# Kernel tuning notes

Measured on AMD Instinct MI355X. Metric: run time of the kernel, lower is better.

Reference implementation:

```python
import jax, jax.numpy as jnp
import numpy as np

B, TQ, TK = 4, 256, 256
Q, K, H = 256, 256, 256


def setup_inputs() -> dict:
    key = jax.random.key(0)
    ks = jax.random.split(key, 10)
    s = 0.05
    return {
        "queries": jax.random.normal(ks[0], (B, TQ, Q), dtype=jnp.float32),
        "keys": jax.random.normal(ks[1], (B, TK, K), dtype=jnp.float32),
        # lengths in [T//2, T] so no fully-masked query rows (torch would NaN there too)
        "query_lengths": jax.random.randint(ks[2], (B,), TQ // 2, TQ + 1),
        "key_lengths": jax.random.randint(ks[3], (B,), TK // 2, TK + 1),
        # nn.Linear(Q+K, H): weight applied as x @ W1; torch concat order is [keys, queries]
        "W1": jax.random.normal(ks[4], (K + Q, H), dtype=jnp.float32) * s,
        "b1": jax.random.normal(ks[5], (H,), dtype=jnp.float32) * s,
        "W2": jax.random.normal(ks[6], (H, H), dtype=jnp.float32) * s,
        "b2": jax.random.normal(ks[7], (H,), dtype=jnp.float32) * s,
        "W3": jax.random.normal(ks[8], (H, 1), dtype=jnp.float32) * s,
        "b3": jax.random.normal(ks[9], (1,), dtype=jnp.float32) * s,
    }


def reference(queries, keys, query_lengths, key_lengths, W1, b1, W2, b2, W3, b3):
    Bn, Tq, Qd = queries.shape
    Tk, Kd = keys.shape[1], keys.shape[2]
    # Split the first linear: concat([keys, queries]) @ W1 == keys@W1[:K] + queries@W1[K:]
    kh = jnp.einsum("bkd,dh->bkh", keys, W1[:Kd])      # [B,Tk,H]
    qh = jnp.einsum("bqd,dh->bqh", queries, W1[Kd:])   # [B,Tq,H]
    h = jax.nn.relu(qh[:, :, None, :] + kh[:, None, :, :] + b1)  # [B,Tq,Tk,H]
    h = jax.nn.relu(jnp.einsum("bqkh,hg->bqkg", h, W2) + b2)     # [B,Tq,Tk,H]
    scores = jnp.einsum("bqkh,h->bqk", h, W3[:, 0]) + b3[0]       # [B,Tq,Tk]
    # mask True where position is padding (query OR key out of range)
    mask = (jnp.arange(Tq)[None, :, None] >= query_lengths[:, None, None]) | (
        jnp.arange(Tk)[None, None, :] >= key_lengths[:, None, None]
    )
    scores = jnp.where(mask, -1e30, scores)
    probs = jax.nn.softmax(scores, axis=-1)
    probs = jnp.where(mask, 0.0, probs)
    return jnp.einsum("bqk,bkd->bqd", probs, keys)  # [B,Tq,K]
```

## Files before the change

### kernel.cpp

```cpp
#include <hip/hip_runtime.h>
#include <cstdint>

#define BATCH 4
#define TQ 256
#define TK 256
#define DIM 256
#define HD 256

typedef _Float16 f16x8 __attribute__((ext_vector_type(8)));
typedef float f32x4 __attribute__((ext_vector_type(4)));

union U4H8 { uint4 u; f16x8 v; };

#define KEEP(x) asm volatile("" : "+v"(x))

__device__ __forceinline__ unsigned short f2h(float f) {
    _Float16 h = (_Float16)f;
    unsigned short u;
    __builtin_memcpy(&u, &h, 2);
    return u;
}

__device__ __forceinline__ uint32_t pk2h(float a, float b) {
    auto r = __builtin_amdgcn_cvt_pkrtz(a, b);
    uint32_t w;
    __builtin_memcpy(&w, &r, 4);
    return w;
}

__global__ __launch_bounds__(256) void prep_all(
    const float* __restrict__ queries, const float* __restrict__ keys,
    const float* __restrict__ W1, const float* __restrict__ b1,
    const float* __restrict__ W2,
    float* __restrict__ qh, float* __restrict__ kh,
    unsigned short* __restrict__ W2T) {
    int i = blockIdx.x;
    int t = threadIdx.x;
    if (i >= 512) {
        __shared__ float tile[32][33];
        int bi = i - 512;
        int tx = t & 31, ty = t >> 5;
        int tc = (bi & 7) * 32, tn = (bi >> 3) * 32;
#pragma unroll
        for (int r = 0; r < 4; ++r)
            tile[ty + r * 8][tx] = W2[(tc + ty + r * 8) * HD + tn + tx];
        __syncthreads();
#pragma unroll
        for (int r = 0; r < 4; ++r)
            W2T[(tn + ty + r * 8) * HD + tc + tx] = f2h(tile[tx][ty + r * 8]);
        return;
    }
    bool isQ = i < 256;
    int r0 = (i & 255) * 4;
    const float* X = isQ ? queries : keys;
    const float* W = W1 + (isQ ? DIM * HD : 0);
    float* O = isQ ? qh : kh;
    __shared__ float4 xs4[4][DIM / 4];
    xs4[t >> 6][t & 63] =
        *(const float4*)(X + (size_t)(r0 + (t >> 6)) * DIM + (t & 63) * 4);
    __syncthreads();
    float acc[4] = {0.f, 0.f, 0.f, 0.f};
#pragma unroll 4
    for (int d4 = 0; d4 < DIM / 4; ++d4) {
        const float4 x0 = xs4[0][d4];
        const float4 x1 = xs4[1][d4];
        const float4 x2 = xs4[2][d4];
        const float4 x3 = xs4[3][d4];
        const float w0 = W[(d4 * 4 + 0) * HD + t];
        const float w1 = W[(d4 * 4 + 1) * HD + t];
        const float w2 = W[(d4 * 4 + 2) * HD + t];
        const float w3 = W[(d4 * 4 + 3) * HD + t];
        acc[0] = fmaf(x0.x, w0, acc[0]); acc[1] = fmaf(x1.x, w0, acc[1]);
        acc[2] = fmaf(x2.x, w0, acc[2]); acc[3] = fmaf(x3.x, w0, acc[3]);
        acc[0] = fmaf(x0.y, w1, acc[0]); acc[1] = fmaf(x1.y, w1, acc[1]);
        acc[2] = fmaf(x2.y, w1, acc[2]); acc[3] = fmaf(x3.y, w1, acc[3]);
        acc[0] = fmaf(x0.z, w2, acc[0]); acc[1] = fmaf(x1.z, w2, acc[1]);
        acc[2] = fmaf(x2.z, w2, acc[2]); acc[3] = fmaf(x3.z, w2, acc[3]);
        acc[0] = fmaf(x0.w, w3, acc[0]); acc[1] = fmaf(x1.w, w3, acc[1]);
        acc[2] = fmaf(x2.w, w3, acc[2]); acc[3] = fmaf(x3.w, w3, acc[3]);
    }
    float bias = isQ ? b1[t] : 0.f;
#pragma unroll
    for (int r = 0; r < 4; ++r) O[(size_t)(r0 + r) * HD + t] = acc[r] + bias;
}

__global__ __launch_bounds__(256, 2) void mlp_attn(
    const float* __restrict__ qh, const float* __restrict__ kh,
    const unsigned short* __restrict__ W2T,
    const float* __restrict__ b2, const float* __restrict__ W3,
    const float* __restrict__ keys,
    const int* __restrict__ qlens, const int* __restrict__ klens,
    float* __restrict__ out) {
    int orig = blockIdx.x;
    int task = ((orig & 7) << 6) | (orig >> 3);
    int b = task & 3;
    int q0 = (task >> 2) << 1;
    int t = threadIdx.x;
    int qlen = qlens[b];
    float* orow = out + (b * TQ + q0) * DIM;
    if (q0 >= qlen) { orow[t] = 0.f; orow[DIM + t] = 0.f; return; }
    bool v1 = (q0 + 1) < qlen;
    int klen = klens[b];
    int nch = (klen + 31) >> 5;

    __shared__ uint4 Afrag[2][8][4][64];
    __shared__ float sprt[4][2][TK];
    __shared__ float srow[2][TK];
    __shared__ float Qlds[2][HD];
    __shared__ float red[16];

    int w = t >> 6, lane = t & 63;
    int col = lane & 15, quad = lane >> 4;

    int nb = w << 6;
    uint4 bfr[4][8];
#pragma unroll
    for (int nt = 0; nt < 4; ++nt) {
        int n = nb + (nt << 4) + col;
        const uint4* r = (const uint4*)(W2T + n * HD) + quad;
#pragma unroll
        for (int s = 0; s < 8; ++s) bfr[nt][s] = r[s * 4];
    }
    float b2v[4][4], w3v[4][4];
#pragma unroll
    for (int nt = 0; nt < 4; ++nt)
#pragma unroll
        for (int r = 0; r < 4; ++r) {
            int n = nb + (nt << 4) + (quad << 2) + r;
            b2v[nt][r] = b2[n];
            w3v[nt][r] = W3[n];
        }

    int qsel = w >> 1;
    int rsub = ((w & 1) << 4) | col;
    const float* kbase = kh + (b * TK + rsub) * HD + (quad << 3);

    {
        const float* qrowg = qh + (b * TQ + q0 + qsel) * HD + (quad << 3);
        const float* krow = kbase;
        uint4* as = &Afrag[0][0][w][lane];
#pragma unroll
        for (int s = 0; s < 8; ++s) {
            const float4 k0 = *(const float4*)(krow + s * 32);
            const float4 k1 = *(const float4*)(krow + s * 32 + 4);
            const float4 qa = *(const float4*)(qrowg + s * 32);
            const float4 qb = *(const float4*)(qrowg + s * 32 + 4);
            uint4 wv;
            wv.x = pk2h(fmaxf(k0.x + qa.x, 0.f), fmaxf(k0.y + qa.y, 0.f));
            wv.y = pk2h(fmaxf(k0.z + qa.z, 0.f), fmaxf(k0.w + qa.w, 0.f));
            wv.z = pk2h(fmaxf(k1.x + qb.x, 0.f), fmaxf(k1.y + qb.y, 0.f));
            wv.w = pk2h(fmaxf(k1.z + qb.z, 0.f), fmaxf(k1.w + qb.w, 0.f));
            as[s * 256] = wv;
        }
    }
    Qlds[0][t] = qh[(b * TQ + q0) * HD + t];
    Qlds[1][t] = qh[(b * TQ + q0 + 1) * HD + t];

#pragma unroll
    for (int nt = 0; nt < 4; ++nt)
#pragma unroll
        for (int s = 0; s < 8; ++s) {
            KEEP(bfr[nt][s].x); KEEP(bfr[nt][s].y);
            KEEP(bfr[nt][s].z); KEEP(bfr[nt][s].w);
        }

    __syncthreads();

    auto sloop = [&](int cur, int mt, f32x4* acc) {
#pragma unroll
        for (int s = 0; s < 8; ++s) {
            U4H8 au;
            au.u = Afrag[cur][s][mt][lane];
#pragma unroll
            for (int nt = 0; nt < 4; ++nt) {
                U4H8 bu;
                bu.u = bfr[nt][s];
                acc[nt] = __builtin_amdgcn_mfma_f32_16x16x32_f16(
                    bu.v, au.v, acc[nt], 0, 0, 0);
            }
        }
    };
    auto epi = [&](int c, int mt, const f32x4* acc) {
        int hf = mt >> 1, m2 = mt & 1;
        float part = 0.f;
#pragma unroll
        for (int nt = 0; nt < 4; ++nt)
#pragma unroll
            for (int r = 0; r < 4; ++r)
                part = fmaf(fmaxf(acc[nt][r] + b2v[nt][r], 0.f), w3v[nt][r], part);
        part += __shfl_xor(part, 16, 64);
        part += __shfl_xor(part, 32, 64);
        if (quad == 0)
            sprt[w][hf][(c << 5) | (m2 << 4) | col] = part;
    };

    for (int c = 0; c < nch; ++c) {
        int cur = c & 1;
        bool stg = (c + 1 < nch);
        const float* krow = kbase + (((c + 1) << 5)) * HD;
        uint4* as1 = &Afrag[cur ^ 1][0][w][lane];

        auto wslot = [&](int s, const float4& k0, const float4& k1) {
            const float4 qa = *(const float4*)&Qlds[qsel][s * 32 + (quad << 3)];
            const float4 qb = *(const float4*)&Qlds[qsel][s * 32 + (quad << 3) + 4];
            uint4 wv;
            wv.x = pk2h(fmaxf(k0.x + qa.x, 0.f), fmaxf(k0.y + qa.y, 0.f));
            wv.y = pk2h(fmaxf(k0.z + qa.z, 0.f), fmaxf(k0.w + qa.w, 0.f));
            wv.z = pk2h(fmaxf(k1.x + qb.x, 0.f), fmaxf(k1.y + qb.y, 0.f));
            wv.w = pk2h(fmaxf(k1.z + qb.z, 0.f), fmaxf(k1.w + qb.w, 0.f));
            as1[s * 256] = wv;
        };

        float4 A0, A1, A2, A3, B0, B1, B2, B3;
        if (stg) {
            A0 = *(const float4*)(krow);       A1 = *(const float4*)(krow + 4);
            A2 = *(const float4*)(krow + 32);  A3 = *(const float4*)(krow + 36);
        }
        __builtin_amdgcn_sched_barrier(0);

        {
            f32x4 acc[4] = {};
            sloop(cur, 0, acc);
            if (stg) {
                wslot(0, A0, A1); wslot(1, A2, A3);
                B0 = *(const float4*)(krow + 64);  B1 = *(const float4*)(krow + 68);
                B2 = *(const float4*)(krow + 96);  B3 = *(const float4*)(krow + 100);
            }
            __builtin_amdgcn_sched_barrier(0);
            epi(c, 0, acc);
            if (stg) {
                wslot(2, B0, B1); wslot(3, B2, B3);
                A0 = *(const float4*)(krow + 128); A1 = *(const float4*)(krow + 132);
                A2 = *(const float4*)(krow + 160); A3 = *(const float4*)(krow + 164);
            }
            __builtin_amdgcn_sched_barrier(0);
        }
        {
            f32x4 acc[4] = {};
            sloop(cur, 1, acc);
            if (stg) {
                wslot(4, A0, A1); wslot(5, A2, A3);
                B0 = *(const float4*)(krow + 192); B1 = *(const float4*)(krow + 196);
                B2 = *(const float4*)(krow + 224); B3 = *(const float4*)(krow + 228);
            }
            __builtin_amdgcn_sched_barrier(0);
            epi(c, 1, acc);
            if (stg) { wslot(6, B0, B1); wslot(7, B2, B3); }
        }
        {
            f32x4 acc[4] = {};
            sloop(cur, 2, acc);
            epi(c, 2, acc);
        }
        {
            f32x4 acc[4] = {};
            sloop(cur, 3, acc);
            epi(c, 3, acc);
        }
        __syncthreads();
    }

    float s0 = -3.4e38f, s1 = -3.4e38f;
    if (t < klen) {
        s0 = (sprt[0][0][t] + sprt[1][0][t]) + (sprt[2][0][t] + sprt[3][0][t]);
        s1 = (sprt[0][1][t] + sprt[1][1][t]) + (sprt[2][1][t] + sprt[3][1][t]);
    }
    float m0 = s0, m1 = s1;
#pragma unroll
    for (int off = 1; off < 64; off <<= 1) {
        m0 = fmaxf(m0, __shfl_xor(m0, off, 64));
        m1 = fmaxf(m1, __shfl_xor(m1, off, 64));
    }
    if (lane == 0) { red[w] = m0; red[8 + w] = m1; }
    __syncthreads();
    m0 = fmaxf(fmaxf(red[0], red[1]), fmaxf(red[2], red[3]));
    m1 = fmaxf(fmaxf(red[8], red[9]), fmaxf(red[10], red[11]));
    float e0 = (t < klen) ? __expf(s0 - m0) : 0.f;
    float e1 = (t < klen) ? __expf(s1 - m1) : 0.f;
    float u0 = e0, u1 = e1;
#pragma unroll
    for (int off = 1; off < 64; off <<= 1) {
        u0 += __shfl_xor(u0, off, 64);
        u1 += __shfl_xor(u1, off, 64);
    }
    if (lane == 0) { red[4 + w] = u0; red[12 + w] = u1; }
    __syncthreads();
    float d0 = red[4] + red[5] + red[6] + red[7];
    float d1 = red[12] + red[13] + red[14] + red[15];
    srow[0][t] = e0 / d0;
    srow[1][t] = e1 / d1;
    __syncthreads();

    float a0 = 0.f, a1 = 0.f;
    const float* kp = keys + b * TK * DIM + t;
#pragma unroll 16
    for (int k = 0; k < klen; ++k) {
        float v = kp[k * DIM];
        a0 = fmaf(srow[0][k], v, a0);
        a1 = fmaf(srow[1][k], v, a1);
    }
    orow[t] = a0;
    orow[DIM + t] = v1 ? a1 : 0.f;
}

extern "C" void kernel_launch(void* const* d_in, const int* in_sizes, int n_in,
                              void* d_out, int out_size, void* d_ws, size_t ws_size,
                              hipStream_t stream) {
    (void)in_sizes; (void)n_in; (void)out_size; (void)ws_size;
    const float* queries = (const float*)d_in[0];
    const float* keys    = (const float*)d_in[1];
    const int*   qlens   = (const int*)d_in[2];
    const int*   klens   = (const int*)d_in[3];
    const float* W1      = (const float*)d_in[4];
    const float* b1      = (const float*)d_in[5];
    const float* W2      = (const float*)d_in[6];
    const float* b2      = (const float*)d_in[7];
    const float* W3      = (const float*)d_in[8];
    float* out = (float*)d_out;

    float* qh = (float*)d_ws;
    float* kh = qh + BATCH * TQ * HD;
    unsigned short* W2T = (unsigned short*)(kh + BATCH * TK * HD);

    prep_all<<<576, 256, 0, stream>>>(queries, keys, W1, b1, W2, qh, kh, W2T);
    mlp_attn<<<BATCH * TQ / 2, 256, 0, stream>>>(
        qh, kh, W2T, b2, W3, keys, qlens, klens, out);
}
```

Measured before the change: 128.1 us.

## Store qh/kh in fp16, single-buffer A fragments with packed half relu

The prep kernel now writes the query and key projections as fp16 instead of fp32, halving workspace traffic. In the main kernel the first-layer sum and relu run as packed half-precision vector ops. The A-fragment LDS buffer drops from double to single buffering, and the next chunk is written after an extra barrier instead of interleaved with the MFMA work. This saves LDS and register pressure, but it serializes fragment staging with compute and rounds qh and kh before the add, not after.

Result: faster. 125.5 us (-2.0%).

```diff
diff --git a/kernel.cpp b/kernel.cpp
--- a/kernel.cpp
+++ b/kernel.cpp
@@ -21,18 +21,22 @@
     return u;
 }
 
-__device__ __forceinline__ uint32_t pk2h(float a, float b) {
-    auto r = __builtin_amdgcn_cvt_pkrtz(a, b);
-    uint32_t w;
-    __builtin_memcpy(&w, &r, 4);
-    return w;
+__device__ __forceinline__ f16x8 relu8(f16x8 h) {
+    f16x8 z = {};
+#if __has_builtin(__builtin_elementwise_max)
+    return __builtin_elementwise_max(h, z);
+#else
+#pragma unroll
+    for (int i = 0; i < 8; ++i) h[i] = h[i] > (_Float16)0 ? h[i] : (_Float16)0;
+    return h;
+#endif
 }
 
 __global__ __launch_bounds__(256) void prep_all(
     const float* __restrict__ queries, const float* __restrict__ keys,
     const float* __restrict__ W1, const float* __restrict__ b1,
     const float* __restrict__ W2,
-    float* __restrict__ qh, float* __restrict__ kh,
+    unsigned short* __restrict__ qhh, unsigned short* __restrict__ khh,
     unsigned short* __restrict__ W2T) {
     int i = blockIdx.x;
     int t = threadIdx.x;
@@ -54,7 +58,7 @@
     int r0 = (i & 255) * 4;
     const float* X = isQ ? queries : keys;
     const float* W = W1 + (isQ ? DIM * HD : 0);
-    float* O = isQ ? qh : kh;
+    unsigned short* O = isQ ? qhh : khh;
     __shared__ float4 xs4[4][DIM / 4];
     xs4[t >> 6][t & 63] =
         *(const float4*)(X + (size_t)(r0 + (t >> 6)) * DIM + (t & 63) * 4);
@@ -81,11 +85,12 @@
     }
     float bias = isQ ? b1[t] : 0.f;
 #pragma unroll
-    for (int r = 0; r < 4; ++r) O[(size_t)(r0 + r) * HD + t] = acc[r] + bias;
+    for (int r = 0; r < 4; ++r)
+        O[(size_t)(r0 + r) * HD + t] = f2h(acc[r] + bias);
 }
 
 __global__ __launch_bounds__(256, 2) void mlp_attn(
-    const float* __restrict__ qh, const float* __restrict__ kh,
+    const unsigned short* __restrict__ qh, const unsigned short* __restrict__ kh,
     const unsigned short* __restrict__ W2T,
     const float* __restrict__ b2, const float* __restrict__ W3,
     const float* __restrict__ keys,
@@ -103,10 +108,10 @@
     int klen = klens[b];
     int nch = (klen + 31) >> 5;
 
-    __shared__ uint4 Afrag[2][8][4][64];
+    __shared__ uint4 Afrag[8][4][64];
     __shared__ float sprt[4][2][TK];
     __shared__ float srow[2][TK];
-    __shared__ float Qlds[2][HD];
+    __shared__ uint4 qbuf4[2][HD / 8];
     __shared__ float red[16];
 
     int w = t >> 6, lane = t & 63;
@@ -133,28 +138,24 @@
 
     int qsel = w >> 1;
     int rsub = ((w & 1) << 4) | col;
-    const float* kbase = kh + (b * TK + rsub) * HD + (quad << 3);
+    const unsigned short* kbase = kh + (b * TK + rsub) * HD + (quad << 3);
+
+    if (t < 64)
+        qbuf4[t >> 5][t & 31] =
+            *(const uint4*)(qh + (size_t)(b * TQ + q0 + (t >> 5)) * HD + (t & 31) * 8);
 
     {
-        const float* qrowg = qh + (b * TQ + q0 + qsel) * HD + (quad << 3);
-        const float* krow = kbase;
-        uint4* as = &Afrag[0][0][w][lane];
+        const unsigned short* qrowg = qh + (b * TQ + q0 + qsel) * HD + (quad << 3);
+        uint4* as = &Afrag[0][w][lane];
 #pragma unroll
         for (int s = 0; s < 8; ++s) {
-            const float4 k0 = *(const float4*)(krow + s * 32);
-            const float4 k1 = *(const float4*)(krow + s * 32 + 4);
-            const float4 qa = *(const float4*)(qrowg + s * 32);
-            const float4 qb = *(const float4*)(qrowg + s * 32 + 4);
-            uint4 wv;
-            wv.x = pk2h(fmaxf(k0.x + qa.x, 0.f), fmaxf(k0.y + qa.y, 0.f));
-            wv.y = pk2h(fmaxf(k0.z + qa.z, 0.f), fmaxf(k0.w + qa.w, 0.f));
-            wv.z = pk2h(fmaxf(k1.x + qb.x, 0.f), fmaxf(k1.y + qb.y, 0.f));
-            wv.w = pk2h(fmaxf(k1.z + qb.z, 0.f), fmaxf(k1.w + qb.w, 0.f));
-            as[s * 256] = wv;
-        }
-    }
-    Qlds[0][t] = qh[(b * TQ + q0) * HD + t];
-    Qlds[1][t] = qh[(b * TQ + q0 + 1) * HD + t];
+            U4H8 kf, qf, h;
+            kf.u = *(const uint4*)(kbase + s * 32);
+            qf.u = *(const uint4*)(qrowg + s * 32);
+            h.v = relu8(kf.v + qf.v);
+            as[s * 256] = h.u;
+        }
+    }
 
 #pragma unroll
     for (int nt = 0; nt < 4; ++nt)
@@ -166,11 +167,11 @@
 
     __syncthreads();
 
-    auto sloop = [&](int cur, int mt, f32x4* acc) {
+    auto sloop = [&](int mt, f32x4* acc) {
 #pragma unroll
         for (int s = 0; s < 8; ++s) {
             U4H8 au;
-            au.u = Afrag[cur][s][mt][lane];
+            au.u = Afrag[s][mt][lane];
 #pragma unroll
             for (int nt = 0; nt < 4; ++nt) {
                 U4H8 bu;
@@ -195,67 +196,35 @@
     };
 
     for (int c = 0; c < nch; ++c) {
-        int cur = c & 1;
         bool stg = (c + 1 < nch);
-        const float* krow = kbase + (((c + 1) << 5)) * HD;
-        uint4* as1 = &Afrag[cur ^ 1][0][w][lane];
-
-        auto wslot = [&](int s, const float4& k0, const float4& k1) {
-            const float4 qa = *(const float4*)&Qlds[qsel][s * 32 + (quad << 3)];
-            const float4 qb = *(const float4*)&Qlds[qsel][s * 32 + (quad << 3) + 4];
-            uint4 wv;
-            wv.x = pk2h(fmaxf(k0.x + qa.x, 0.f), fmaxf(k0.y + qa.y, 0.f));
-            wv.y = pk2h(fmaxf(k0.z + qa.z, 0.f), fmaxf(k0.w + qa.w, 0.f));
-            wv.z = pk2h(fmaxf(k1.x + qb.x, 0.f), fmaxf(k1.y + qb.y, 0.f));
-            wv.w = pk2h(fmaxf(k1.z + qb.z, 0.f), fmaxf(k1.w + qb.w, 0.f));
-            as1[s * 256] = wv;
-        };
-
-        float4 A0, A1, A2, A3, B0, B1, B2, B3;
+        const unsigned short* krow = kbase + (((c + 1) << 5)) * HD;
+        uint4 Kst[8];
         if (stg) {
-            A0 = *(const float4*)(krow);       A1 = *(const float4*)(krow + 4);
-            A2 = *(const float4*)(krow + 32);  A3 = *(const float4*)(krow + 36);
+#pragma unroll
+            for (int s = 0; s < 8; ++s) Kst[s] = *(const uint4*)(krow + s * 32);
+#pragma unroll
+            for (int s = 0; s < 8; ++s) {
+                KEEP(Kst[s].x); KEEP(Kst[s].y); KEEP(Kst[s].z); KEEP(Kst[s].w);
+            }
         }
         __builtin_amdgcn_sched_barrier(0);
 
-        {
-            f32x4 acc[4] = {};
-            sloop(cur, 0, acc);
-            if (stg) {
-                wslot(0, A0, A1); wslot(1, A2, A3);
-                B0 = *(const float4*)(krow + 64);  B1 = *(const float4*)(krow + 68);
-                B2 = *(const float4*)(krow + 96);  B3 = *(const float4*)(krow + 100);
+        {   f32x4 acc[4] = {}; sloop(0, acc); epi(c, 0, acc); }
+        {   f32x4 acc[4] = {}; sloop(1, acc); epi(c, 1, acc); }
+        {   f32x4 acc[4] = {}; sloop(2, acc); epi(c, 2, acc); }
+        {   f32x4 acc[4] = {}; sloop(3, acc); epi(c, 3, acc); }
+
+        __syncthreads();
+        if (stg) {
+            uint4* as = &Afrag[0][w][lane];
+#pragma unroll
+            for (int s = 0; s < 8; ++s) {
+                U4H8 kf, qf, h;
+                kf.u = Kst[s];
+                qf.u = qbuf4[qsel][s * 4 + quad];
+                h.v = relu8(kf.v + qf.v);
+                as[s * 256] = h.u;
             }
-            __builtin_amdgcn_sched_barrier(0);
-            epi(c, 0, acc);
-            if (stg) {
-                wslot(2, B0, B1); wslot(3, B2, B3);
-                A0 = *(const float4*)(krow + 128); A1 = *(const float4*)(krow + 132);
-                A2 = *(const float4*)(krow + 160); A3 = *(const float4*)(krow + 164);
-            }
-            __builtin_amdgcn_sched_barrier(0);
-        }
-        {
-            f32x4 acc[4] = {};
-            sloop(cur, 1, acc);
-            if (stg) {
-                wslot(4, A0, A1); wslot(5, A2, A3);
-                B0 = *(const float4*)(krow + 192); B1 = *(const float4*)(krow + 196);
-                B2 = *(const float4*)(krow + 224); B3 = *(const float4*)(krow + 228);
-            }
-            __builtin_amdgcn_sched_barrier(0);
-            epi(c, 1, acc);
-            if (stg) { wslot(6, B0, B1); wslot(7, B2, B3); }
-        }
-        {
-            f32x4 acc[4] = {};
-            sloop(cur, 2, acc);
-            epi(c, 2, acc);
-        }
-        {
-            f32x4 acc[4] = {};
-            sloop(cur, 3, acc);
-            epi(c, 3, acc);
         }
         __syncthreads();
     }
@@ -318,11 +287,11 @@
     const float* W3      = (const float*)d_in[8];
     float* out = (float*)d_out;
 
-    float* qh = (float*)d_ws;
-    float* kh = qh + BATCH * TQ * HD;
-    unsigned short* W2T = (unsigned short*)(kh + BATCH * TK * HD);
-
-    prep_all<<<576, 256, 0, stream>>>(queries, keys, W1, b1, W2, qh, kh, W2T);
+    unsigned short* qhh = (unsigned short*)d_ws;
+    unsigned short* khh = qhh + BATCH * TQ * HD;
+    unsigned short* W2T = khh + BATCH * TK * HD;
+
+    prep_all<<<576, 256, 0, stream>>>(queries, keys, W1, b1, W2, qhh, khh, W2T);
     mlp_attn<<<BATCH * TQ / 2, 256, 0, stream>>>(
-        qh, kh, W2T, b2, W3, keys, qlens, klens, out);
-}
+        qhh, khh, W2T, b2, W3, keys, qlens, klens, out);
+}
```
